# Kernel optimization log

Hardware: AMD Instinct MI355X
Metric: run time of the kernel (lower is better)

The kernel has to match this reference:

```python
import jax, jax.numpy as jnp
import numpy as np

N, C, OUT, E, H = 4096, 256, 256, 131072, 8
DH = C // H
EPS = 1e-5


def layer_norm(h, g, b):
    mu = jnp.mean(h, axis=-1, keepdims=True)
    var = jnp.mean(jnp.square(h - mu), axis=-1, keepdims=True)
    return (h - mu) * jax.lax.rsqrt(var + EPS) * g + b


def setup_inputs() -> dict:
    key = jax.random.key(0)
    ks = jax.random.split(key, 12)
    s = 1.0 / np.sqrt(C)
    return {
        "x": jax.random.normal(ks[0], (N, C), jnp.float32),
        "edge_index": jax.random.randint(ks[1], (2, E), 0, N, jnp.int32),
        "edge_attr": jax.random.normal(ks[2], (E, C), jnp.float32),
        # nn.MultiheadAttention params
        "in_proj_w": jax.random.uniform(ks[3], (3 * C, C), jnp.float32, -s, s),
        "in_proj_b": jnp.zeros((3 * C,), jnp.float32),
        "attn_out_w": jax.random.uniform(ks[4], (C, C), jnp.float32, -s, s),
        "attn_out_b": jnp.zeros((C,), jnp.float32),
        # edge_mlp: Linear(3C -> OUT) + LayerNorm(OUT)
        "edge_w": jax.random.uniform(ks[5], (OUT, 3 * C), jnp.float32, -1 / np.sqrt(3 * C), 1 / np.sqrt(3 * C)),
        "edge_b": jax.random.uniform(ks[6], (OUT,), jnp.float32, -1 / np.sqrt(3 * C), 1 / np.sqrt(3 * C)),
        "ln1_g": jnp.ones((OUT,), jnp.float32),
        "ln1_b": jnp.zeros((OUT,), jnp.float32),
        # output_proj: Linear(C + OUT -> OUT)
        "out_w": jax.random.uniform(ks[7], (OUT, C + OUT), jnp.float32, -1 / np.sqrt(C + OUT), 1 / np.sqrt(C + OUT)),
        "out_b": jax.random.uniform(ks[8], (OUT,), jnp.float32, -1 / np.sqrt(C + OUT), 1 / np.sqrt(C + OUT)),
        "ln2_g": jnp.ones((OUT,), jnp.float32),
        "ln2_b": jnp.zeros((OUT,), jnp.float32),
    }


def reference(x, edge_index, edge_attr, in_proj_w, in_proj_b, attn_out_w, attn_out_b,
              edge_w, edge_b, ln1_g, ln1_b, out_w, out_b, ln2_g, ln2_b):
    num_nodes = x.shape[0]
    # --- dense self-attention over all nodes (seq len = N, batch 1) ---
    qkv = x @ in_proj_w.T + in_proj_b            # [N, 3C]
    q, k, v = jnp.split(qkv, 3, axis=-1)
    q = q.reshape(num_nodes, H, DH).transpose(1, 0, 2)  # [H, N, DH]
    k = k.reshape(num_nodes, H, DH).transpose(1, 0, 2)
    v = v.reshape(num_nodes, H, DH).transpose(1, 0, 2)
    scores = jnp.einsum("hqd,hkd->hqk", q, k) / np.sqrt(DH)
    attn = jax.nn.softmax(scores, axis=-1)       # dropout inactive at eval
    ctx = jnp.einsum("hqk,hkd->hqd", attn, v)    # [H, N, DH]
    ctx = ctx.transpose(1, 0, 2).reshape(num_nodes, C)
    x_attn = ctx @ attn_out_w.T + attn_out_b     # [N, C]
    # --- vectorized edge messages: gather -> MLP -> scatter-add ---
    row, col = edge_index[0], edge_index[1]
    msg_in = jnp.concatenate([x[row], x[col], edge_attr], axis=-1)  # [E, 3C]
    msg = jax.nn.relu(layer_norm(msg_in @ edge_w.T + edge_b, ln1_g, ln1_b))
    node_messages = jax.ops.segment_sum(msg, col, num_segments=num_nodes)  # [N, OUT]
    # --- combine, project, residual, norm ---
    combined = jnp.concatenate([x_attn, node_messages], axis=-1)
    out = combined @ out_w.T + out_b
    out = out + x                                # OUT == C so residual fires
    return layer_norm(out, ln2_g, ln2_b)
```

## Files before the change

### kernel.cpp

```cpp
#include <hip/hip_runtime.h>
#include <hip/hip_bf16.h>
#include <math.h>

typedef __bf16 bf16;
typedef __bf16 bf16x8 __attribute__((ext_vector_type(8)));
typedef __bf16 bf16x4 __attribute__((ext_vector_type(4)));
typedef float f32x4 __attribute__((ext_vector_type(4)));

#define MFMA16(a, b, c) __builtin_amdgcn_mfma_f32_16x16x32_bf16((a), (b), (c), 0, 0, 0)

#define N_NODES 4096
#define C_DIM   256
#define E_EDGES 131072
#define APAD    280

__device__ __forceinline__ float ldf(const void* p, int i, bool f32) {
    return f32 ? ((const float*)p)[i] : (float)((const bf16*)p)[i];
}

__device__ __forceinline__ bf16x8 ld8(const void* base, size_t off, bool f32) {
    if (f32) {
        const float* p = (const float*)base + off;
        float4 a = *(const float4*)p;
        float4 b = *(const float4*)(p + 4);
        bf16x8 r;
        r[0] = (bf16)a.x; r[1] = (bf16)a.y; r[2] = (bf16)a.z; r[3] = (bf16)a.w;
        r[4] = (bf16)b.x; r[5] = (bf16)b.y; r[6] = (bf16)b.z; r[7] = (bf16)b.w;
        return r;
    }
    return *(const bf16x8*)((const bf16*)base + off);
}

__global__ __launch_bounds__(64) void detect_dtype(const void* x, int* flag)
{
    const bf16* xb = (const bf16*)x;
    int tid = threadIdx.x;
    int bad = 0;
    for (int i = tid; i < 4096; i += 64) {
        float v = fabsf((float)xb[i]);
        if (!(v >= 1e-6f && v <= 100.0f)) bad++;
    }
#pragma unroll
    for (int m = 1; m < 64; m <<= 1) bad += __shfl_xor(bad, m);
    if (tid == 0) *flag = (bad > 400) ? 1 : 0;
}

__global__ __launch_bounds__(256) void convert_inputs(
    const void* s0, const void* s1, const void* s2, const void* s3, const void* s4,
    bf16* dst, const int* flag)
{
    int idx = blockIdx.x * 256 + threadIdx.x;
    const void* src; int local;
    if (idx < 1048576)      { src = s0; local = idx; }
    else if (idx < 1245184) { src = s1; local = idx - 1048576; }
    else if (idx < 1310720) { src = s2; local = idx - 1245184; }
    else if (idx < 1507328) { src = s3; local = idx - 1310720; }
    else                    { src = s4; local = idx - 1507328; }
    if (*flag) dst[idx] = (bf16)(((const float*)src)[local]);
    else ((unsigned short*)dst)[idx] = ((const unsigned short*)src)[local];
}

__global__ __launch_bounds__(256) void edge_hist(
    const int* __restrict__ ecol, int* __restrict__ counts)
{
    int e = blockIdx.x * 256 + threadIdx.x;
    atomicAdd(&counts[ecol[e]], 1);
}

__global__ __launch_bounds__(256) void edge_scan(
    const int* __restrict__ counts, int* __restrict__ offsets,
    int* __restrict__ cursor)
{
    __shared__ int part[256];
    __shared__ int pref[257];
    int t = threadIdx.x;
    int base = t * 16;
    int s = 0;
#pragma unroll
    for (int i = 0; i < 16; ++i) s += counts[base + i];
    part[t] = s;
    __syncthreads();
    if (t == 0) {
        int run = 0;
        for (int i = 0; i < 256; ++i) { pref[i] = run; run += part[i]; }
        pref[256] = run;
    }
    __syncthreads();
    int off = pref[t];
#pragma unroll
    for (int i = 0; i < 16; ++i) {
        offsets[base + i] = off;
        cursor[base + i]  = off;
        off += counts[base + i];
    }
    if (t == 255) offsets[4096] = off;
}

__global__ __launch_bounds__(256) void edge_scatter(
    const int* __restrict__ ecol, int* __restrict__ cursor,
    int* __restrict__ eid)
{
    int e = blockIdx.x * 256 + threadIdx.x;
    int pos = atomicAdd(&cursor[ecol[e]], 1);
    eid[pos] = e;
}

__global__ __launch_bounds__(256) void gemm_bt(
    const bf16* __restrict__ A, int lda,
    const bf16* __restrict__ W, int ldw,
    const void* __restrict__ bias,
    void* __restrict__ Cout, int ldc, int c_f32,
    const bf16* __restrict__ resid, int ldr,
    int K, const int* __restrict__ flag)
{
    const bool f32 = (*flag != 0);
    const int wave = threadIdx.x >> 6;
    const int lane = threadIdx.x & 63;
    const int quad = lane >> 4;
    const int l16  = lane & 15;
    const int m_base = blockIdx.x * 32;
    const int n_base = blockIdx.y * 256 + wave * 64;

    const bf16* a0p = A + (size_t)(m_base + l16) * lda + quad * 8;
    const bf16* a1p = a0p + (size_t)16 * lda;
    const bf16* wp  = W + (size_t)(n_base + l16) * ldw + quad * 8;

    f32x4 acc[2][4] = {};
    for (int k = 0; k < K; k += 32) {
        bf16x8 a0 = *(const bf16x8*)(a0p + k);
        bf16x8 a1 = *(const bf16x8*)(a1p + k);
#pragma unroll
        for (int nt = 0; nt < 4; ++nt) {
            bf16x8 b = *(const bf16x8*)(wp + (size_t)nt * 16 * ldw + k);
            acc[0][nt] = MFMA16(a0, b, acc[0][nt]);
            acc[1][nt] = MFMA16(a1, b, acc[1][nt]);
        }
    }
#pragma unroll
    for (int mt = 0; mt < 2; ++mt) {
#pragma unroll
        for (int nt = 0; nt < 4; ++nt) {
            int col = n_base + nt * 16 + l16;
            float bv = bias ? ldf(bias, col, f32) : 0.0f;
#pragma unroll
            for (int r = 0; r < 4; ++r) {
                int row = m_base + mt * 16 + quad * 4 + r;
                float v = acc[mt][nt][r] + bv;
                if (resid) v += (float)resid[(size_t)row * ldr + col];
                if (c_f32) ((float*)Cout)[(size_t)row * ldc + col] = v;
                else       ((bf16*)Cout)[(size_t)row * ldc + col] = (bf16)v;
            }
        }
    }
}

__global__ __launch_bounds__(256) void transpose_v(
    const bf16* __restrict__ qkv, bf16* __restrict__ vt)
{
    __shared__ bf16 t[32][65];
    const int n0 = blockIdx.x * 64;
    const int c0 = blockIdx.y * 32;
    const int tid = threadIdx.x;
    {
        int cl = tid & 31, nl = tid >> 5;
#pragma unroll
        for (int p = 0; p < 8; ++p) {
            int n = nl + p * 8;
            t[cl][n] = qkv[(size_t)(n0 + n) * 768 + 512 + c0 + cl];
        }
    }
    __syncthreads();
    {
        int nn = tid & 63, cc = tid >> 6;
#pragma unroll
        for (int p = 0; p < 8; ++p) {
            int c = cc + p * 4;
            vt[(size_t)(c0 + c) * 4096 + n0 + nn] = t[c][nn];
        }
    }
}

__global__ __launch_bounds__(256) void attn_kernel(
    const bf16* __restrict__ qkv,
    const bf16* __restrict__ vt,
    bf16* __restrict__ ctx)
{
    __shared__ bf16 P[4][16][32];
    __shared__ float mL[4][16], lL[4][16];
    __shared__ float oL[4][16][32];
    const int tid  = threadIdx.x;
    const int wave = tid >> 6;
    const int lane = tid & 63;
    const int quad = lane >> 4;
    const int l16  = lane & 15;
    const int h  = blockIdx.x >> 8;
    const int qt = blockIdx.x & 255;

    const float csc = 1.4426950408889634f * 0.17677669529663687f;

    bf16x8 qf = *(const bf16x8*)(qkv + (size_t)(qt * 16 + l16) * 768 + h * 32 + quad * 8);
    const bf16* kcol = qkv + 256 + h * 32 + quad * 8;
    const bf16* vth  = vt + (size_t)h * 32 * 4096;

    float mrun[4] = {-INFINITY, -INFINITY, -INFINITY, -INFINITY};
    float lrun[4] = {0.f, 0.f, 0.f, 0.f};
    f32x4 o0 = {}, o1 = {};
    const f32x4 zero = {};

    const int kbeg = wave * 1024;
    for (int k0 = kbeg; k0 < kbeg + 1024; k0 += 32) {
        const bf16* kp = kcol + (size_t)(k0 + l16) * 768;
        bf16x8 kf0 = *(const bf16x8*)kp;
        bf16x8 kf1 = *(const bf16x8*)(kp + (size_t)16 * 768);
        f32x4 s0 = MFMA16(qf, kf0, zero);
        f32x4 s1 = MFMA16(qf, kf1, zero);

        float tm[4], p0[4], p1[4], ts[4], alpha[4], nm[4];
#pragma unroll
        for (int r = 0; r < 4; ++r) tm[r] = fmaxf(s0[r], s1[r]);
#pragma unroll
        for (int msk = 1; msk < 16; msk <<= 1) {
#pragma unroll
            for (int r = 0; r < 4; ++r) tm[r] = fmaxf(tm[r], __shfl_xor(tm[r], msk));
        }
#pragma unroll
        for (int r = 0; r < 4; ++r) {
            nm[r] = fmaxf(mrun[r], tm[r]);
            alpha[r] = exp2f((mrun[r] - nm[r]) * csc);
            p0[r] = exp2f((s0[r] - nm[r]) * csc);
            p1[r] = exp2f((s1[r] - nm[r]) * csc);
            ts[r] = p0[r] + p1[r];
        }
#pragma unroll
        for (int msk = 1; msk < 16; msk <<= 1) {
#pragma unroll
            for (int r = 0; r < 4; ++r) ts[r] += __shfl_xor(ts[r], msk);
        }
#pragma unroll
        for (int r = 0; r < 4; ++r) {
            lrun[r] = lrun[r] * alpha[r] + ts[r];
            mrun[r] = nm[r];
            o0[r] *= alpha[r];
            o1[r] *= alpha[r];
        }
        __syncthreads();
#pragma unroll
        for (int r = 0; r < 4; ++r) {
            P[wave][quad * 4 + r][l16]      = (bf16)p0[r];
            P[wave][quad * 4 + r][16 + l16] = (bf16)p1[r];
        }
        __syncthreads();
        bf16x8 pf = *(const bf16x8*)&P[wave][l16][quad * 8];
        const bf16* vp = vth + (size_t)l16 * 4096 + k0 + quad * 8;
        bf16x8 v0 = *(const bf16x8*)vp;
        bf16x8 v1 = *(const bf16x8*)(vp + (size_t)16 * 4096);
        o0 = MFMA16(pf, v0, o0);
        o1 = MFMA16(pf, v1, o1);
    }
    if (l16 == 0) {
#pragma unroll
        for (int r = 0; r < 4; ++r) {
            mL[wave][quad * 4 + r] = mrun[r];
            lL[wave][quad * 4 + r] = lrun[r];
        }
    }
#pragma unroll
    for (int r = 0; r < 4; ++r) {
        oL[wave][quad * 4 + r][l16]      = o0[r];
        oL[wave][quad * 4 + r][16 + l16] = o1[r];
    }
    __syncthreads();
    if (wave == 0) {
#pragma unroll
        for (int r = 0; r < 4; ++r) {
            int row = quad * 4 + r;
            float m0 = mL[0][row], m1 = mL[1][row], m2 = mL[2][row], m3 = mL[3][row];
            float ms = fmaxf(fmaxf(m0, m1), fmaxf(m2, m3));
            float f0 = exp2f((m0 - ms) * csc), f1 = exp2f((m1 - ms) * csc);
            float f2 = exp2f((m2 - ms) * csc), f3 = exp2f((m3 - ms) * csc);
            float ls = lL[0][row] * f0 + lL[1][row] * f1 + lL[2][row] * f2 + lL[3][row] * f3;
            float inv = 1.0f / ls;
            float a = (oL[0][row][l16] * f0 + oL[1][row][l16] * f1 +
                       oL[2][row][l16] * f2 + oL[3][row][l16] * f3) * inv;
            float b = (oL[0][row][16 + l16] * f0 + oL[1][row][16 + l16] * f1 +
                       oL[2][row][16 + l16] * f2 + oL[3][row][16 + l16] * f3) * inv;
            bf16* cp = ctx + (size_t)(qt * 16 + row) * 256 + h * 32;
            cp[l16]      = (bf16)a;
            cp[16 + l16] = (bf16)b;
        }
    }
}

__global__ __launch_bounds__(256) void edge_msg_v3(
    const int* __restrict__ erow, const int* __restrict__ ecol,
    const void* __restrict__ eattr,
    const bf16* __restrict__ ew,
    const void* __restrict__ eb,
    const void* __restrict__ g1, const void* __restrict__ b1,
    const bf16* __restrict__ U, const bf16* __restrict__ V,
    bf16* __restrict__ msg, const int* __restrict__ flag)
{
    __shared__ char smem[64 * APAD * 2];
    bf16* Asm = (bf16*)smem;
    float (*Trow)[256] = (float(*)[256])smem;

    const bool f32 = (*flag != 0);
    const int tid  = threadIdx.x;
    const int wave = tid >> 6;
    const int lane = tid & 63;
    const int quad = lane >> 4;
    const int l16  = lane & 15;
    const int e_base = blockIdx.x * 64;

    bf16x8 breg[8][4];
#pragma unroll
    for (int k0 = 0; k0 < 8; ++k0)
#pragma unroll
        for (int nt = 0; nt < 4; ++nt)
            breg[k0][nt] = *(const bf16x8*)(ew +
                (size_t)(wave * 64 + nt * 16 + l16) * 768 + 512 + k0 * 32 + quad * 8);

    {
        int row   = tid >> 2;
        int cbase = (tid & 3) * 64;
        bf16* dst = Asm + row * APAD + cbase;
        if (!f32) {
            const bf16* src = (const bf16*)eattr + (size_t)(e_base + row) * 256 + cbase;
#pragma unroll
            for (int j = 0; j < 8; ++j)
                *(bf16x8*)(dst + j * 8) = *(const bf16x8*)(src + j * 8);
        } else {
            const float* src = (const float*)eattr + (size_t)(e_base + row) * 256 + cbase;
#pragma unroll
            for (int j = 0; j < 8; ++j) {
                float4 a = *(const float4*)(src + j * 8);
                float4 b = *(const float4*)(src + j * 8 + 4);
                bf16x8 r;
                r[0] = (bf16)a.x; r[1] = (bf16)a.y; r[2] = (bf16)a.z; r[3] = (bf16)a.w;
                r[4] = (bf16)b.x; r[5] = (bf16)b.y; r[6] = (bf16)b.z; r[7] = (bf16)b.w;
                *(bf16x8*)(dst + j * 8) = r;
            }
        }
    }
    __syncthreads();

    f32x4 acc[4][4] = {};
#pragma unroll
    for (int k0 = 0; k0 < 8; ++k0) {
#pragma unroll
        for (int mt = 0; mt < 4; ++mt) {
            bf16x8 af = *(const bf16x8*)(Asm + (mt * 16 + l16) * APAD + k0 * 32 + quad * 8);
#pragma unroll
            for (int nt = 0; nt < 4; ++nt)
                acc[mt][nt] = MFMA16(af, breg[k0][nt], acc[mt][nt]);
        }
    }

    float ebv[4];
#pragma unroll
    for (int nt = 0; nt < 4; ++nt)
        ebv[nt] = ldf(eb, wave * 64 + nt * 16 + l16, f32);
    float glv[4], blv[4];
#pragma unroll
    for (int i = 0; i < 4; ++i) {
        glv[i] = ldf(g1, lane * 4 + i, f32);
        blv[i] = ldf(b1, lane * 4 + i, f32);
    }

    for (int p = 0; p < 2; ++p) {
        __syncthreads();
#pragma unroll
        for (int mtl = 0; mtl < 2; ++mtl) {
            int mt = p * 2 + mtl;
#pragma unroll
            for (int nt = 0; nt < 4; ++nt)
#pragma unroll
                for (int r = 0; r < 4; ++r)
                    Trow[mtl * 16 + quad * 4 + r][wave * 64 + nt * 16 + l16] =
                        acc[mt][nt][r] + ebv[nt];
        }
        __syncthreads();
        for (int rl = 0; rl < 8; ++rl) {
            int row = wave * 8 + rl;
            int e = e_base + p * 32 + row;
            int er = erow[e], ec = ecol[e];
            float4 t4 = *(const float4*)&Trow[row][lane * 4];
            bf16x4 u4 = *(const bf16x4*)(U + (size_t)er * 256 + lane * 4);
            bf16x4 w4 = *(const bf16x4*)(V + (size_t)ec * 256 + lane * 4);
            float v[4];
            v[0] = t4.x + (float)u4[0] + (float)w4[0];
            v[1] = t4.y + (float)u4[1] + (float)w4[1];
            v[2] = t4.z + (float)u4[2] + (float)w4[2];
            v[3] = t4.w + (float)u4[3] + (float)w4[3];
            float s = v[0] + v[1] + v[2] + v[3];
            float q = v[0]*v[0] + v[1]*v[1] + v[2]*v[2] + v[3]*v[3];
#pragma unroll
            for (int msk = 1; msk < 64; msk <<= 1) {
                s += __shfl_xor(s, msk);
                q += __shfl_xor(q, msk);
            }
            float mean = s * (1.0f / 256.0f);
            float var  = q * (1.0f / 256.0f) - mean * mean;
            float rstd = rsqrtf(var + 1e-5f);
            bf16x4 o;
#pragma unroll
            for (int i = 0; i < 4; ++i)
                o[i] = (bf16)fmaxf((v[i] - mean) * rstd * glv[i] + blv[i], 0.0f);
            *(bf16x4*)(msg + (size_t)e * 256 + lane * 4) = o;
        }
    }
}

__global__ __launch_bounds__(256) void node_gather(
    const bf16* __restrict__ msg,
    const int* __restrict__ offsets, const int* __restrict__ eid,
    bf16* __restrict__ combined)
{
    const int wave = threadIdx.x >> 6, lane = threadIdx.x & 63;
    const int node = blockIdx.x * 4 + wave;
    const int start = offsets[node];
    const int cnt   = offsets[node + 1] - start;
    float a0 = 0.f, a1 = 0.f, a2 = 0.f, a3 = 0.f;
    int i = 0;
    for (; i + 4 <= cnt; i += 4) {
        int e0 = eid[start + i],     e1 = eid[start + i + 1];
        int e2 = eid[start + i + 2], e3 = eid[start + i + 3];
        bf16x4 r0 = *(const bf16x4*)(msg + (size_t)e0 * 256 + lane * 4);
        bf16x4 r1 = *(const bf16x4*)(msg + (size_t)e1 * 256 + lane * 4);
        bf16x4 r2 = *(const bf16x4*)(msg + (size_t)e2 * 256 + lane * 4);
        bf16x4 r3 = *(const bf16x4*)(msg + (size_t)e3 * 256 + lane * 4);
        a0 += (float)r0[0] + (float)r1[0] + (float)r2[0] + (float)r3[0];
        a1 += (float)r0[1] + (float)r1[1] + (float)r2[1] + (float)r3[1];
        a2 += (float)r0[2] + (float)r1[2] + (float)r2[2] + (float)r3[2];
        a3 += (float)r0[3] + (float)r1[3] + (float)r2[3] + (float)r3[3];
    }
    for (; i < cnt; ++i) {
        int e = eid[start + i];
        bf16x4 r = *(const bf16x4*)(msg + (size_t)e * 256 + lane * 4);
        a0 += (float)r[0]; a1 += (float)r[1]; a2 += (float)r[2]; a3 += (float)r[3];
    }
    bf16* cp = combined + (size_t)node * 512 + 256 + lane * 4;
    cp[0] = (bf16)a0; cp[1] = (bf16)a1; cp[2] = (bf16)a2; cp[3] = (bf16)a3;
}

__global__ __launch_bounds__(256) void edge_node(
    const bf16* __restrict__ x,
    const int* __restrict__ erow,
    const void* __restrict__ eattr,
    const bf16* __restrict__ ew,
    const void* __restrict__ eb,
    const void* __restrict__ g1, const void* __restrict__ b1,
    const int* __restrict__ offsets, const int* __restrict__ eid,
    bf16* __restrict__ combined, const int* __restrict__ flag)
{
    __shared__ float part[32][4][2];
    const bool f32 = (*flag != 0);
    const int wave = threadIdx.x >> 6;
    const int lane = threadIdx.x & 63;
    const int quad = lane >> 4;
    const int l16  = lane & 15;
    const int n = blockIdx.x;
    const int start = offsets[n];
    const int cnt   = offsets[n + 1] - start;

    float gv[4], bv[4], ebv[4];
#pragma unroll
    for (int nt = 0; nt < 4; ++nt) {
        int col = wave * 64 + nt * 16 + l16;
        gv[nt]  = ldf(g1, col, f32);
        bv[nt]  = ldf(b1, col, f32);
        ebv[nt] = ldf(eb, col, f32);
    }
    const bf16* wp = ew + (size_t)(wave * 64 + l16) * 768 + quad * 8;
    const bf16* xn = x + (size_t)n * 256 + quad * 8;

    f32x4 acc1[4] = {};
#pragma unroll
    for (int kk = 0; kk < 8; ++kk) {
        bf16x8 a = *(const bf16x8*)(xn + kk * 32);
#pragma unroll
        for (int nt = 0; nt < 4; ++nt) {
            bf16x8 b = *(const bf16x8*)(wp + (size_t)nt * 16 * 768 + 256 + kk * 32);
            acc1[nt] = MFMA16(a, b, acc1[nt]);
        }
    }
    float nacc[4] = {0.f, 0.f, 0.f, 0.f};
    for (int c0 = 0; c0 < cnt; c0 += 32) {
        int i0 = c0 + l16;      i0 = (i0 < cnt) ? i0 : 0;
        int i1 = c0 + 16 + l16; i1 = (i1 < cnt) ? i1 : 0;
        int e0 = eid[start + i0];
        int e1 = eid[start + i1];
        const bf16* xr0 = x + (size_t)erow[e0] * 256 + quad * 8;
        const bf16* xr1 = x + (size_t)erow[e1] * 256 + quad * 8;
        f32x4 acc[2][4];
#pragma unroll
        for (int nt = 0; nt < 4; ++nt) { acc[0][nt] = acc1[nt]; acc[1][nt] = acc1[nt]; }
#pragma unroll
        for (int kk = 0; kk < 8; ++kk) {
            bf16x8 a0 = *(const bf16x8*)(xr0 + kk * 32);
            bf16x8 a1 = *(const bf16x8*)(xr1 + kk * 32);
#pragma unroll
            for (int nt = 0; nt < 4; ++nt) {
                bf16x8 b = *(const bf16x8*)(wp + (size_t)nt * 16 * 768 + kk * 32);
                acc[0][nt] = MFMA16(a0, b, acc[0][nt]);
                acc[1][nt] = MFMA16(a1, b, acc[1][nt]);
            }
        }
#pragma unroll
        for (int kk = 0; kk < 8; ++kk) {
            int koff = quad * 8 + kk * 32;
            bf16x8 a0 = ld8(eattr, (size_t)e0 * 256 + koff, f32);
            bf16x8 a1 = ld8(eattr, (size_t)e1 * 256 + koff, f32);
#pragma unroll
            for (int nt = 0; nt < 4; ++nt) {
                bf16x8 b = *(const bf16x8*)(wp + (size_t)nt * 16 * 768 + 512 + kk * 32);
                acc[0][nt] = MFMA16(a0, b, acc[0][nt]);
                acc[1][nt] = MFMA16(a1, b, acc[1][nt]);
            }
        }
#pragma unroll
        for (int mt = 0; mt < 2; ++mt)
#pragma unroll
            for (int nt = 0; nt < 4; ++nt)
#pragma unroll
                for (int r = 0; r < 4; ++r) acc[mt][nt][r] += ebv[nt];
        float ps[2][4], pq[2][4];
#pragma unroll
        for (int mt = 0; mt < 2; ++mt)
#pragma unroll
            for (int r = 0; r < 4; ++r) {
                float s = 0.f, q = 0.f;
#pragma unroll
                for (int nt = 0; nt < 4; ++nt) {
                    float v = acc[mt][nt][r];
                    s += v; q += v * v;
                }
                ps[mt][r] = s; pq[mt][r] = q;
            }
#pragma unroll
        for (int msk = 1; msk < 16; msk <<= 1)
#pragma unroll
            for (int mt = 0; mt < 2; ++mt)
#pragma unroll
                for (int r = 0; r < 4; ++r) {
                    ps[mt][r] += __shfl_xor(ps[mt][r], msk);
                    pq[mt][r] += __shfl_xor(pq[mt][r], msk);
                }
        if (l16 == 0) {
#pragma unroll
            for (int mt = 0; mt < 2; ++mt)
#pragma unroll
                for (int r = 0; r < 4; ++r) {
                    part[mt * 16 + quad * 4 + r][wave][0] = ps[mt][r];
                    part[mt * 16 + quad * 4 + r][wave][1] = pq[mt][r];
                }
        }
        __syncthreads();
#pragma unroll
        for (int mt = 0; mt < 2; ++mt)
#pragma unroll
            for (int r = 0; r < 4; ++r) {
                int row = mt * 16 + quad * 4 + r;
                float s = part[row][0][0] + part[row][1][0] + part[row][2][0] + part[row][3][0];
                float q = part[row][0][1] + part[row][1][1] + part[row][2][1] + part[row][3][1];
                float mean = s * (1.0f / 256.0f);
                float var  = q * (1.0f / 256.0f) - mean * mean;
                float rstd = rsqrtf(var + 1e-5f);
                if ((c0 + row) < cnt) {
#pragma unroll
                    for (int nt = 0; nt < 4; ++nt) {
                        float val = (acc[mt][nt][r] - mean) * rstd * gv[nt] + bv[nt];
                        nacc[nt] += fmaxf(val, 0.0f);
                    }
                }
            }
        __syncthreads();
    }
#pragma unroll
    for (int nt = 0; nt < 4; ++nt) {
        nacc[nt] += __shfl_xor(nacc[nt], 16);
        nacc[nt] += __shfl_xor(nacc[nt], 32);
    }
    if (quad == 0) {
#pragma unroll
        for (int nt = 0; nt < 4; ++nt)
            combined[(size_t)n * 512 + 256 + wave * 64 + nt * 16 + l16] = (bf16)nacc[nt];
    }
}

__global__ __launch_bounds__(256) void ln_out_kernel(
    const float* __restrict__ pre,
    const void* __restrict__ g, const void* __restrict__ bb,
    void* __restrict__ out, const int* __restrict__ flag)
{
    const bool f32 = (*flag != 0);
    const int wave = threadIdx.x >> 6, lane = threadIdx.x & 63;
    const int row = blockIdx.x * 4 + wave;
    float4 v4 = *(const float4*)(pre + (size_t)row * 256 + lane * 4);
    float v[4] = {v4.x, v4.y, v4.z, v4.w};
    float s  = v[0] + v[1] + v[2] + v[3];
    float sq = v[0]*v[0] + v[1]*v[1] + v[2]*v[2] + v[3]*v[3];
#pragma unroll
    for (int msk = 1; msk < 64; msk <<= 1) {
        s  += __shfl_xor(s, msk);
        sq += __shfl_xor(sq, msk);
    }
    float mean = s * (1.0f / 256.0f);
    float var  = sq * (1.0f / 256.0f) - mean * mean;
    float rstd = rsqrtf(var + 1e-5f);
#pragma unroll
    for (int i = 0; i < 4; ++i) {
        int c = lane * 4 + i;
        float r = (v[i] - mean) * rstd * ldf(g, c, f32) + ldf(bb, c, f32);
        if (f32) ((float*)out)[(size_t)row * 256 + c] = r;
        else     ((bf16*)out)[(size_t)row * 256 + c] = (bf16)r;
    }
}

extern "C" void kernel_launch(void* const* d_in, const int* in_sizes, int n_in,
                              void* d_out, int out_size, void* d_ws, size_t ws_size,
                              hipStream_t stream)
{
    const void* x_raw  = d_in[0];
    const int*  eidx   = (const int*)d_in[1];
    const void* eattr  = d_in[2];
    const void* in_w   = d_in[3];
    const void* in_b   = d_in[4];
    const void* ao_w   = d_in[5];
    const void* ao_b   = d_in[6];
    const void* e_w    = d_in[7];
    const void* e_b    = d_in[8];
    const void* g1     = d_in[9];
    const void* b1     = d_in[10];
    const void* o_w    = d_in[11];
    const void* o_b    = d_in[12];
    const void* g2     = d_in[13];
    const void* b2     = d_in[14];

    char* ws = (char*)d_ws;
    bf16*  qkv      = (bf16*)(ws);
    bf16*  vt       = (bf16*)(ws + 6291456);
    bf16*  ctx      = (bf16*)(ws + 8388608);
    bf16*  combined = (bf16*)(ws + 10485760);
    int*   counts   = (int*)(ws + 14680064);
    int*   offsets  = (int*)(ws + 14696448);
    int*   cursor   = (int*)(ws + 14712848);
    int*   eid      = (int*)(ws + 14729232);
    float* out_pre  = (float*)(ws + 18874368);
    bf16*  U        = (bf16*)(ws + 18874368);
    bf16*  V        = (bf16*)(ws + 20971520);
    bf16*  canon    = (bf16*)(ws + 23068672);
    int*   flag     = (int*)(ws + 26345472);
    bf16*  msg      = (bf16*)(ws + 26345728);

    const size_t WS_NEEDED = 93454592;

    bf16* x_bf   = canon;
    bf16* inw_bf = canon + 1048576;
    bf16* aow_bf = canon + 1245184;
    bf16* ew_bf  = canon + 1310720;
    bf16* ow_bf  = canon + 1507328;

    const int* erow = eidx;
    const int* ecol = eidx + E_EDGES;

    detect_dtype<<<dim3(1), 64, 0, stream>>>(x_raw, flag);
    convert_inputs<<<dim3(6400), 256, 0, stream>>>(x_raw, in_w, ao_w, e_w, o_w,
                                                   canon, flag);
    hipMemsetAsync(counts, 0, 16384, stream);
    edge_hist<<<dim3(E_EDGES / 256), 256, 0, stream>>>(ecol, counts);
    edge_scan<<<dim3(1), 256, 0, stream>>>(counts, offsets, cursor);
    edge_scatter<<<dim3(E_EDGES / 256), 256, 0, stream>>>(ecol, cursor, eid);

    gemm_bt<<<dim3(128, 1), 256, 0, stream>>>(x_bf, 256, ew_bf, 768, nullptr,
                                              U, 256, 0, nullptr, 0, 256, flag);
    gemm_bt<<<dim3(128, 1), 256, 0, stream>>>(x_bf, 256, ew_bf + 256, 768, nullptr,
                                              V, 256, 0, nullptr, 0, 256, flag);

    gemm_bt<<<dim3(128, 3), 256, 0, stream>>>(x_bf, 256, inw_bf, 256, in_b,
                                              qkv, 768, 0, nullptr, 0, 256, flag);
    transpose_v<<<dim3(64, 8), 256, 0, stream>>>(qkv, vt);
    attn_kernel<<<dim3(2048), 256, 0, stream>>>(qkv, vt, ctx);
    gemm_bt<<<dim3(128, 1), 256, 0, stream>>>(ctx, 256, aow_bf, 256, ao_b,
                                              combined, 512, 0, nullptr, 0, 256, flag);
    if (ws_size >= WS_NEEDED) {
        edge_msg_v3<<<dim3(E_EDGES / 64), 256, 0, stream>>>(erow, ecol, eattr,
                                                            ew_bf, e_b, g1, b1,
                                                            U, V, msg, flag);
        node_gather<<<dim3(N_NODES / 4), 256, 0, stream>>>(msg, offsets, eid, combined);
    } else {
        edge_node<<<dim3(N_NODES), 256, 0, stream>>>(x_bf, erow, eattr,
                                                     ew_bf, e_b, g1, b1,
                                                     offsets, eid, combined, flag);
    }
    gemm_bt<<<dim3(128, 1), 256, 0, stream>>>(combined, 512, ow_bf, 512, o_b,
                                              out_pre, 256, 1, x_bf, 256, 512, flag);
    ln_out_kernel<<<dim3(N_NODES / 4), 256, 0, stream>>>(out_pre, g2, b2, d_out, flag);
}
```

Measured before the change: 557.0 us.

## Restructure attention inner loop with 64-key steps, K prefetch, lazy rescale, swizzled P

The flash-attention loop now handles 64 keys per iteration and prefetches the next K fragments one step ahead. The row-sum reduction is deferred to the end of the loop, and the rescale is skipped unless the running max grows. Both __syncthreads in the loop are removed in favour of a per-wave XOR-swizzled LDS buffer for P, and the V transpose writes a permuted key order so the P layout matches the MFMA operand. Together these aim to cut barrier stalls, shuffle traffic and exp work. The cost is more register pressure, plus a reliance on wave-synchronous LDS access with no explicit barrier.

Result: faster. 539.6 us (-3.1%).

```diff
diff --git a/kernel.cpp b/kernel.cpp
--- a/kernel.cpp
+++ b/kernel.cpp
@@ -172,10 +172,11 @@
     __syncthreads();
     {
         int nn = tid & 63, cc = tid >> 6;
+        int np = ((nn & 15) << 2) | (nn >> 4);
 #pragma unroll
         for (int p = 0; p < 8; ++p) {
             int c = cc + p * 4;
-            vt[(size_t)(c0 + c) * 4096 + n0 + nn] = t[c][nn];
+            vt[(size_t)(c0 + c) * 4096 + n0 + np] = t[c][nn];
         }
     }
 }
@@ -185,7 +186,7 @@
     const bf16* __restrict__ vt,
     bf16* __restrict__ ctx)
 {
-    __shared__ bf16 P[4][16][32];
+    __shared__ char Psm[4][2048];
     __shared__ float mL[4][16], lL[4][16];
     __shared__ float oL[4][16][32];
     const int tid  = threadIdx.x;
@@ -200,68 +201,102 @@
 
     bf16x8 qf = *(const bf16x8*)(qkv + (size_t)(qt * 16 + l16) * 768 + h * 32 + quad * 8);
     const bf16* kcol = qkv + 256 + h * 32 + quad * 8;
-    const bf16* vth  = vt + (size_t)h * 32 * 4096;
-
-    float mrun[4] = {-INFINITY, -INFINITY, -INFINITY, -INFINITY};
-    float lrun[4] = {0.f, 0.f, 0.f, 0.f};
+    const bf16* vth  = vt + (size_t)(h * 32) * 4096;
+
+    char* Pw = Psm[wave];
+    char* pst[4];
+#pragma unroll
+    for (int r = 0; r < 4; ++r) {
+        int row = quad * 4 + r;
+        pst[r] = Pw + row * 128 + ((l16 * 8) ^ ((row & 7) << 4));
+    }
+    const char* prd0 = Pw + l16 * 128 + (((0 * 64) + quad * 16) ^ ((l16 & 7) << 4));
+    const char* prd1 = Pw + l16 * 128 + (((1 * 64) + quad * 16) ^ ((l16 & 7) << 4));
+
+    float mrun[4], lacc[4];
+#pragma unroll
+    for (int r = 0; r < 4; ++r) { mrun[r] = -INFINITY; lacc[r] = 0.f; }
     f32x4 o0 = {}, o1 = {};
     const f32x4 zero = {};
 
     const int kbeg = wave * 1024;
-    for (int k0 = kbeg; k0 < kbeg + 1024; k0 += 32) {
-        const bf16* kp = kcol + (size_t)(k0 + l16) * 768;
-        bf16x8 kf0 = *(const bf16x8*)kp;
-        bf16x8 kf1 = *(const bf16x8*)(kp + (size_t)16 * 768);
-        f32x4 s0 = MFMA16(qf, kf0, zero);
-        f32x4 s1 = MFMA16(qf, kf1, zero);
-
-        float tm[4], p0[4], p1[4], ts[4], alpha[4], nm[4];
-#pragma unroll
-        for (int r = 0; r < 4; ++r) tm[r] = fmaxf(s0[r], s1[r]);
-#pragma unroll
-        for (int msk = 1; msk < 16; msk <<= 1) {
-#pragma unroll
-            for (int r = 0; r < 4; ++r) tm[r] = fmaxf(tm[r], __shfl_xor(tm[r], msk));
-        }
+    bf16x8 kf[4];
+#pragma unroll
+    for (int t = 0; t < 4; ++t)
+        kf[t] = *(const bf16x8*)(kcol + (size_t)(kbeg + t * 16 + l16) * 768);
+
+    for (int k0 = kbeg; k0 < kbeg + 1024; k0 += 64) {
+        bf16x8 vf00 = *(const bf16x8*)(vth + (size_t)l16 * 4096 + k0 + quad * 8);
+        bf16x8 vf01 = *(const bf16x8*)(vth + (size_t)(16 + l16) * 4096 + k0 + quad * 8);
+        bf16x8 vf10 = *(const bf16x8*)(vth + (size_t)l16 * 4096 + k0 + 32 + quad * 8);
+        bf16x8 vf11 = *(const bf16x8*)(vth + (size_t)(16 + l16) * 4096 + k0 + 32 + quad * 8);
+
+        f32x4 s0 = MFMA16(qf, kf[0], zero);
+        f32x4 s1 = MFMA16(qf, kf[1], zero);
+        f32x4 s2 = MFMA16(qf, kf[2], zero);
+        f32x4 s3 = MFMA16(qf, kf[3], zero);
+
+        if (k0 + 64 < kbeg + 1024) {
+#pragma unroll
+            for (int t = 0; t < 4; ++t)
+                kf[t] = *(const bf16x8*)(kcol + (size_t)(k0 + 64 + t * 16 + l16) * 768);
+        }
+
+        float tm[4];
+#pragma unroll
+        for (int r = 0; r < 4; ++r)
+            tm[r] = fmaxf(fmaxf(s0[r], s1[r]), fmaxf(s2[r], s3[r]));
+#pragma unroll
+        for (int msk = 1; msk < 16; msk <<= 1)
+#pragma unroll
+            for (int r = 0; r < 4; ++r)
+                tm[r] = fmaxf(tm[r], __shfl_xor(tm[r], msk));
+
+        int grow = (tm[0] > mrun[0]) | (tm[1] > mrun[1]) |
+                   (tm[2] > mrun[2]) | (tm[3] > mrun[3]);
+        if (__any(grow)) {
+#pragma unroll
+            for (int r = 0; r < 4; ++r) {
+                float nm = fmaxf(mrun[r], tm[r]);
+                float al = exp2f((mrun[r] - nm) * csc);
+                mrun[r] = nm;
+                lacc[r] *= al;
+                o0[r] *= al;
+                o1[r] *= al;
+            }
+        }
+
 #pragma unroll
         for (int r = 0; r < 4; ++r) {
-            nm[r] = fmaxf(mrun[r], tm[r]);
-            alpha[r] = exp2f((mrun[r] - nm[r]) * csc);
-            p0[r] = exp2f((s0[r] - nm[r]) * csc);
-            p1[r] = exp2f((s1[r] - nm[r]) * csc);
-            ts[r] = p0[r] + p1[r];
-        }
-#pragma unroll
-        for (int msk = 1; msk < 16; msk <<= 1) {
-#pragma unroll
-            for (int r = 0; r < 4; ++r) ts[r] += __shfl_xor(ts[r], msk);
-        }
-#pragma unroll
-        for (int r = 0; r < 4; ++r) {
-            lrun[r] = lrun[r] * alpha[r] + ts[r];
-            mrun[r] = nm[r];
-            o0[r] *= alpha[r];
-            o1[r] *= alpha[r];
-        }
-        __syncthreads();
-#pragma unroll
-        for (int r = 0; r < 4; ++r) {
-            P[wave][quad * 4 + r][l16]      = (bf16)p0[r];
-            P[wave][quad * 4 + r][16 + l16] = (bf16)p1[r];
-        }
-        __syncthreads();
-        bf16x8 pf = *(const bf16x8*)&P[wave][l16][quad * 8];
-        const bf16* vp = vth + (size_t)l16 * 4096 + k0 + quad * 8;
-        bf16x8 v0 = *(const bf16x8*)vp;
-        bf16x8 v1 = *(const bf16x8*)(vp + (size_t)16 * 4096);
-        o0 = MFMA16(pf, v0, o0);
-        o1 = MFMA16(pf, v1, o1);
-    }
+            float p0 = exp2f((s0[r] - mrun[r]) * csc);
+            float p1 = exp2f((s1[r] - mrun[r]) * csc);
+            float p2 = exp2f((s2[r] - mrun[r]) * csc);
+            float p3 = exp2f((s3[r] - mrun[r]) * csc);
+            lacc[r] += (p0 + p1) + (p2 + p3);
+            bf16x4 pk;
+            pk[0] = (bf16)p0; pk[1] = (bf16)p1; pk[2] = (bf16)p2; pk[3] = (bf16)p3;
+            *(bf16x4*)pst[r] = pk;
+        }
+
+        bf16x8 pf0 = *(const bf16x8*)prd0;
+        bf16x8 pf1 = *(const bf16x8*)prd1;
+        o0 = MFMA16(pf0, vf00, o0);
+        o1 = MFMA16(pf0, vf01, o1);
+        o0 = MFMA16(pf1, vf10, o0);
+        o1 = MFMA16(pf1, vf11, o1);
+    }
+
+#pragma unroll
+    for (int msk = 1; msk < 16; msk <<= 1)
+#pragma unroll
+        for (int r = 0; r < 4; ++r)
+            lacc[r] += __shfl_xor(lacc[r], msk);
+
     if (l16 == 0) {
 #pragma unroll
         for (int r = 0; r < 4; ++r) {
             mL[wave][quad * 4 + r] = mrun[r];
-            lL[wave][quad * 4 + r] = lrun[r];
+            lL[wave][quad * 4 + r] = lacc[r];
         }
     }
 #pragma unroll
```

## Rewrite attention with 32x32 MFMA and register-resident P; restructure edge LayerNorm epilogue

Applied to the files above, without the earlier changes.

The attention kernel now uses 32x32x16 bf16 MFMA tiles over 32 queries per block. It computes S transposed so the softmax row reduction needs only one cross-half shuffle. P is packed and exchanged with v_permlane32_swap in registers instead of going through LDS with two block barriers per iteration, and the max is rescaled lazily only when it grows. The edge-message epilogue now has 8 threads per edge row with vectorized 8-wide loads and a 3-step shuffle reduction, using a padded staging tile to avoid LDS bank conflicts. These changes rely on gfx950-specific instructions and exact lane-layout assumptions.

Result: faster. 522.0 us (-6.3%).

```diff
diff --git a/kernel.cpp b/kernel.cpp
--- a/kernel.cpp
+++ b/kernel.cpp
@@ -6,13 +6,16 @@
 typedef __bf16 bf16x8 __attribute__((ext_vector_type(8)));
 typedef __bf16 bf16x4 __attribute__((ext_vector_type(4)));
 typedef float f32x4 __attribute__((ext_vector_type(4)));
+typedef float f32x16 __attribute__((ext_vector_type(16)));
 
 #define MFMA16(a, b, c) __builtin_amdgcn_mfma_f32_16x16x32_bf16((a), (b), (c), 0, 0, 0)
+#define MFMA32(a, b, c) __builtin_amdgcn_mfma_f32_32x32x16_bf16((a), (b), (c), 0, 0, 0)
 
 #define N_NODES 4096
 #define C_DIM   256
 #define E_EDGES 131072
 #define APAD    280
+#define TPAD    260
 
 __device__ __forceinline__ float ldf(const void* p, int i, bool f32) {
     return f32 ? ((const float*)p)[i] : (float)((const bf16*)p)[i];
@@ -31,6 +34,30 @@
     return *(const bf16x8*)((const bf16*)base + off);
 }
 
+__device__ __forceinline__ void ld8f(const void* base, int off, bool f32, float* o) {
+    if (f32) {
+        float4 a = *(const float4*)((const float*)base + off);
+        float4 b = *(const float4*)((const float*)base + off + 4);
+        o[0] = a.x; o[1] = a.y; o[2] = a.z; o[3] = a.w;
+        o[4] = b.x; o[5] = b.y; o[6] = b.z; o[7] = b.w;
+    } else {
+        bf16x8 r = *(const bf16x8*)((const bf16*)base + off);
+#pragma unroll
+        for (int j = 0; j < 8; ++j) o[j] = (float)r[j];
+    }
+}
+
+__device__ __forceinline__ unsigned cvtpk(float a, float b) {
+    unsigned r;
+    asm("v_cvt_pk_bf16_f32 %0, %1, %2" : "=v"(r) : "v"(a), "v"(b));
+    return r;
+}
+__device__ __forceinline__ void pl32swap(unsigned &a, unsigned &b) {
+    asm volatile("v_permlane32_swap_b32 %0, %1" : "+v"(a), "+v"(b));
+}
+
+union PW { unsigned u[4]; bf16x8 v; };
+
 __global__ __launch_bounds__(64) void detect_dtype(const void* x, int* flag)
 {
     const bf16* xb = (const bf16*)x;
@@ -185,109 +212,103 @@
     const bf16* __restrict__ vt,
     bf16* __restrict__ ctx)
 {
-    __shared__ bf16 P[4][16][32];
-    __shared__ float mL[4][16], lL[4][16];
-    __shared__ float oL[4][16][32];
+    __shared__ float oL[4][32][33];
+    __shared__ float mS[4][32];
+    __shared__ float lS[4][32];
     const int tid  = threadIdx.x;
     const int wave = tid >> 6;
     const int lane = tid & 63;
-    const int quad = lane >> 4;
-    const int l16  = lane & 15;
-    const int h  = blockIdx.x >> 8;
-    const int qt = blockIdx.x & 255;
+    const int l32  = lane & 31;
+    const int hl   = lane >> 5;
+    const int h  = blockIdx.x >> 7;
+    const int qt = blockIdx.x & 127;
 
     const float csc = 1.4426950408889634f * 0.17677669529663687f;
 
-    bf16x8 qf = *(const bf16x8*)(qkv + (size_t)(qt * 16 + l16) * 768 + h * 32 + quad * 8);
-    const bf16* kcol = qkv + 256 + h * 32 + quad * 8;
-    const bf16* vth  = vt + (size_t)h * 32 * 4096;
-
-    float mrun[4] = {-INFINITY, -INFINITY, -INFINITY, -INFINITY};
-    float lrun[4] = {0.f, 0.f, 0.f, 0.f};
-    f32x4 o0 = {}, o1 = {};
-    const f32x4 zero = {};
+    const bf16* qrow = qkv + (size_t)(qt * 32 + l32) * 768 + h * 32 + hl * 8;
+    bf16x8 qf1 = *(const bf16x8*)qrow;
+    bf16x8 qf2 = *(const bf16x8*)(qrow + 16);
+
+    const bf16* kbp = qkv + 256 + h * 32 + hl * 8;
+    const bf16* vrp = vt + (size_t)(h * 32 + l32) * 4096 + hl * 8;
+
+    float mrun = -INFINITY, msc = -INFINITY, lacc = 0.f;
+    f32x16 oacc = {};
+    const f32x16 z16 = {};
 
     const int kbeg = wave * 1024;
     for (int k0 = kbeg; k0 < kbeg + 1024; k0 += 32) {
-        const bf16* kp = kcol + (size_t)(k0 + l16) * 768;
-        bf16x8 kf0 = *(const bf16x8*)kp;
-        bf16x8 kf1 = *(const bf16x8*)(kp + (size_t)16 * 768);
-        f32x4 s0 = MFMA16(qf, kf0, zero);
-        f32x4 s1 = MFMA16(qf, kf1, zero);
-
-        float tm[4], p0[4], p1[4], ts[4], alpha[4], nm[4];
-#pragma unroll
-        for (int r = 0; r < 4; ++r) tm[r] = fmaxf(s0[r], s1[r]);
-#pragma unroll
-        for (int msk = 1; msk < 16; msk <<= 1) {
-#pragma unroll
-            for (int r = 0; r < 4; ++r) tm[r] = fmaxf(tm[r], __shfl_xor(tm[r], msk));
-        }
-#pragma unroll
-        for (int r = 0; r < 4; ++r) {
-            nm[r] = fmaxf(mrun[r], tm[r]);
-            alpha[r] = exp2f((mrun[r] - nm[r]) * csc);
-            p0[r] = exp2f((s0[r] - nm[r]) * csc);
-            p1[r] = exp2f((s1[r] - nm[r]) * csc);
-            ts[r] = p0[r] + p1[r];
-        }
-#pragma unroll
-        for (int msk = 1; msk < 16; msk <<= 1) {
-#pragma unroll
-            for (int r = 0; r < 4; ++r) ts[r] += __shfl_xor(ts[r], msk);
-        }
-#pragma unroll
-        for (int r = 0; r < 4; ++r) {
-            lrun[r] = lrun[r] * alpha[r] + ts[r];
-            mrun[r] = nm[r];
-            o0[r] *= alpha[r];
-            o1[r] *= alpha[r];
-        }
-        __syncthreads();
-#pragma unroll
-        for (int r = 0; r < 4; ++r) {
-            P[wave][quad * 4 + r][l16]      = (bf16)p0[r];
-            P[wave][quad * 4 + r][16 + l16] = (bf16)p1[r];
-        }
-        __syncthreads();
-        bf16x8 pf = *(const bf16x8*)&P[wave][l16][quad * 8];
-        const bf16* vp = vth + (size_t)l16 * 4096 + k0 + quad * 8;
-        bf16x8 v0 = *(const bf16x8*)vp;
-        bf16x8 v1 = *(const bf16x8*)(vp + (size_t)16 * 4096);
-        o0 = MFMA16(pf, v0, o0);
-        o1 = MFMA16(pf, v1, o1);
-    }
-    if (l16 == 0) {
-#pragma unroll
-        for (int r = 0; r < 4; ++r) {
-            mL[wave][quad * 4 + r] = mrun[r];
-            lL[wave][quad * 4 + r] = lrun[r];
-        }
-    }
-#pragma unroll
-    for (int r = 0; r < 4; ++r) {
-        oL[wave][quad * 4 + r][l16]      = o0[r];
-        oL[wave][quad * 4 + r][16 + l16] = o1[r];
+        const bf16* kp = kbp + (size_t)(k0 + l32) * 768;
+        bf16x8 kf1 = *(const bf16x8*)kp;
+        bf16x8 kf2 = *(const bf16x8*)(kp + 16);
+        bf16x8 vf1 = *(const bf16x8*)(vrp + k0);
+        bf16x8 vf2 = *(const bf16x8*)(vrp + k0 + 16);
+
+        f32x16 s = MFMA32(kf1, qf1, z16);
+        s = MFMA32(kf2, qf2, s);
+
+        float a0 = fmaxf(fmaxf(s[0], s[1]), fmaxf(s[2], s[3]));
+        float a1 = fmaxf(fmaxf(s[4], s[5]), fmaxf(s[6], s[7]));
+        float a2 = fmaxf(fmaxf(s[8], s[9]), fmaxf(s[10], s[11]));
+        float a3 = fmaxf(fmaxf(s[12], s[13]), fmaxf(s[14], s[15]));
+        float tm = fmaxf(fmaxf(a0, a1), fmaxf(a2, a3));
+        tm = fmaxf(tm, __shfl_xor(tm, 32));
+
+        if (__any(tm > mrun)) {
+            float nm = fmaxf(mrun, tm);
+            float nmsc = nm * csc;
+            float al = exp2f(msc - nmsc);
+            mrun = nm; msc = nmsc;
+            lacc *= al;
+#pragma unroll
+            for (int i = 0; i < 16; ++i) oacc[i] *= al;
+        }
+
+        float p[16];
+#pragma unroll
+        for (int i = 0; i < 16; ++i) {
+            p[i] = exp2f(__builtin_fmaf(s[i], csc, -msc));
+            lacc += p[i];
+        }
+
+        unsigned w0 = cvtpk(p[0], p[1]),  w1 = cvtpk(p[2], p[3]);
+        unsigned w2 = cvtpk(p[4], p[5]),  w3 = cvtpk(p[6], p[7]);
+        unsigned w4 = cvtpk(p[8], p[9]),  w5 = cvtpk(p[10], p[11]);
+        unsigned w6 = cvtpk(p[12], p[13]), w7 = cvtpk(p[14], p[15]);
+        pl32swap(w0, w2); pl32swap(w1, w3);
+        pl32swap(w4, w6); pl32swap(w5, w7);
+        PW f1; f1.u[0] = w0; f1.u[1] = w1; f1.u[2] = w2; f1.u[3] = w3;
+        PW f2; f2.u[0] = w4; f2.u[1] = w5; f2.u[2] = w6; f2.u[3] = w7;
+
+        oacc = MFMA32(vf1, f1.v, oacc);
+        oacc = MFMA32(vf2, f2.v, oacc);
+    }
+
+    lacc += __shfl_xor(lacc, 32);
+    if (hl == 0) { mS[wave][l32] = mrun; lS[wave][l32] = lacc; }
+#pragma unroll
+    for (int i = 0; i < 16; ++i) {
+        int d = (i & 3) + 8 * (i >> 2) + 4 * hl;
+        oL[wave][l32][d] = oacc[i];
     }
     __syncthreads();
-    if (wave == 0) {
-#pragma unroll
-        for (int r = 0; r < 4; ++r) {
-            int row = quad * 4 + r;
-            float m0 = mL[0][row], m1 = mL[1][row], m2 = mL[2][row], m3 = mL[3][row];
-            float ms = fmaxf(fmaxf(m0, m1), fmaxf(m2, m3));
-            float f0 = exp2f((m0 - ms) * csc), f1 = exp2f((m1 - ms) * csc);
-            float f2 = exp2f((m2 - ms) * csc), f3 = exp2f((m3 - ms) * csc);
-            float ls = lL[0][row] * f0 + lL[1][row] * f1 + lL[2][row] * f2 + lL[3][row] * f3;
-            float inv = 1.0f / ls;
-            float a = (oL[0][row][l16] * f0 + oL[1][row][l16] * f1 +
-                       oL[2][row][l16] * f2 + oL[3][row][l16] * f3) * inv;
-            float b = (oL[0][row][16 + l16] * f0 + oL[1][row][16 + l16] * f1 +
-                       oL[2][row][16 + l16] * f2 + oL[3][row][16 + l16] * f3) * inv;
-            bf16* cp = ctx + (size_t)(qt * 16 + row) * 256 + h * 32;
-            cp[l16]      = (bf16)a;
-            cp[16 + l16] = (bf16)b;
-        }
+    {
+        int q = tid >> 3, d0 = (tid & 7) * 4;
+        float m0 = mS[0][q], m1 = mS[1][q], m2 = mS[2][q], m3 = mS[3][q];
+        float ms = fmaxf(fmaxf(m0, m1), fmaxf(m2, m3));
+        float f0 = exp2f((m0 - ms) * csc), f1 = exp2f((m1 - ms) * csc);
+        float f2 = exp2f((m2 - ms) * csc), f3 = exp2f((m3 - ms) * csc);
+        float ls = lS[0][q] * f0 + lS[1][q] * f1 + lS[2][q] * f2 + lS[3][q] * f3;
+        float inv = 1.0f / ls;
+        bf16x4 o4;
+#pragma unroll
+        for (int i = 0; i < 4; ++i) {
+            int d = d0 + i;
+            float v = (oL[0][q][d] * f0 + oL[1][q][d] * f1 +
+                       oL[2][q][d] * f2 + oL[3][q][d] * f3) * inv;
+            o4[i] = (bf16)v;
+        }
+        *(bf16x4*)(ctx + (size_t)(qt * 32 + q) * 256 + h * 32 + d0) = o4;
     }
 }
 
@@ -302,7 +323,7 @@
 {
     __shared__ char smem[64 * APAD * 2];
     bf16* Asm = (bf16*)smem;
-    float (*Trow)[256] = (float(*)[256])smem;
+    float (*Trow)[TPAD] = (float(*)[TPAD])smem;
 
     const bool f32 = (*flag != 0);
     const int tid  = threadIdx.x;
@@ -360,12 +381,6 @@
 #pragma unroll
     for (int nt = 0; nt < 4; ++nt)
         ebv[nt] = ldf(eb, wave * 64 + nt * 16 + l16, f32);
-    float glv[4], blv[4];
-#pragma unroll
-    for (int i = 0; i < 4; ++i) {
-        glv[i] = ldf(g1, lane * 4 + i, f32);
-        blv[i] = ldf(b1, lane * 4 + i, f32);
-    }
 
     for (int p = 0; p < 2; ++p) {
         __syncthreads();
@@ -380,33 +395,58 @@
                         acc[mt][nt][r] + ebv[nt];
         }
         __syncthreads();
-        for (int rl = 0; rl < 8; ++rl) {
-            int row = wave * 8 + rl;
+        {
+            int row = tid >> 3;
+            int seg = tid & 7;
             int e = e_base + p * 32 + row;
             int er = erow[e], ec = ecol[e];
-            float4 t4 = *(const float4*)&Trow[row][lane * 4];
-            bf16x4 u4 = *(const bf16x4*)(U + (size_t)er * 256 + lane * 4);
-            bf16x4 w4 = *(const bf16x4*)(V + (size_t)ec * 256 + lane * 4);
-            float v[4];
-            v[0] = t4.x + (float)u4[0] + (float)w4[0];
-            v[1] = t4.y + (float)u4[1] + (float)w4[1];
-            v[2] = t4.z + (float)u4[2] + (float)w4[2];
-            v[3] = t4.w + (float)u4[3] + (float)w4[3];
-            float s = v[0] + v[1] + v[2] + v[3];
-            float q = v[0]*v[0] + v[1]*v[1] + v[2]*v[2] + v[3]*v[3];
-#pragma unroll
-            for (int msk = 1; msk < 64; msk <<= 1) {
+            const float* tr = &Trow[row][seg * 32];
+            const bf16* up = U + (size_t)er * 256 + seg * 32;
+            const bf16* wp = V + (size_t)ec * 256 + seg * 32;
+            float v[32];
+            float s = 0.f, q = 0.f;
+#pragma unroll
+            for (int i = 0; i < 4; ++i) {
+                float4 ta = *(const float4*)(tr + i * 8);
+                float4 tb = *(const float4*)(tr + i * 8 + 4);
+                bf16x8 u8 = *(const bf16x8*)(up + i * 8);
+                bf16x8 w8 = *(const bf16x8*)(wp + i * 8);
+                float t0 = ta.x + (float)u8[0] + (float)w8[0];
+                float t1 = ta.y + (float)u8[1] + (float)w8[1];
+                float t2 = ta.z + (float)u8[2] + (float)w8[2];
+                float t3 = ta.w + (float)u8[3] + (float)w8[3];
+                float t4 = tb.x + (float)u8[4] + (float)w8[4];
+                float t5 = tb.y + (float)u8[5] + (float)w8[5];
+                float t6 = tb.z + (float)u8[6] + (float)w8[6];
+                float t7 = tb.w + (float)u8[7] + (float)w8[7];
+                v[i*8+0] = t0; v[i*8+1] = t1; v[i*8+2] = t2; v[i*8+3] = t3;
+                v[i*8+4] = t4; v[i*8+5] = t5; v[i*8+6] = t6; v[i*8+7] = t7;
+                s += ((t0 + t1) + (t2 + t3)) + ((t4 + t5) + (t6 + t7));
+                q = __builtin_fmaf(t0, t0, q); q = __builtin_fmaf(t1, t1, q);
+                q = __builtin_fmaf(t2, t2, q); q = __builtin_fmaf(t3, t3, q);
+                q = __builtin_fmaf(t4, t4, q); q = __builtin_fmaf(t5, t5, q);
+                q = __builtin_fmaf(t6, t6, q); q = __builtin_fmaf(t7, t7, q);
+            }
+#pragma unroll
+            for (int msk = 1; msk < 8; msk <<= 1) {
                 s += __shfl_xor(s, msk);
                 q += __shfl_xor(q, msk);
             }
             float mean = s * (1.0f / 256.0f);
             float var  = q * (1.0f / 256.0f) - mean * mean;
             float rstd = rsqrtf(var + 1e-5f);
-            bf16x4 o;
-#pragma unroll
-            for (int i = 0; i < 4; ++i)
-                o[i] = (bf16)fmaxf((v[i] - mean) * rstd * glv[i] + blv[i], 0.0f);
-            *(bf16x4*)(msg + (size_t)e * 256 + lane * 4) = o;
+            bf16* op = msg + (size_t)e * 256 + seg * 32;
+#pragma unroll
+            for (int i = 0; i < 4; ++i) {
+                float gv[8], bv[8];
+                ld8f(g1, seg * 32 + i * 8, f32, gv);
+                ld8f(b1, seg * 32 + i * 8, f32, bv);
+                bf16x8 o8;
+#pragma unroll
+                for (int j = 0; j < 8; ++j)
+                    o8[j] = (bf16)fmaxf((v[i*8+j] - mean) * rstd * gv[j] + bv[j], 0.0f);
+                *(bf16x8*)(op + i * 8) = o8;
+            }
         }
     }
 }
@@ -680,7 +720,7 @@
     gemm_bt<<<dim3(128, 3), 256, 0, stream>>>(x_bf, 256, inw_bf, 256, in_b,
                                               qkv, 768, 0, nullptr, 0, 256, flag);
     transpose_v<<<dim3(64, 8), 256, 0, stream>>>(qkv, vt);
-    attn_kernel<<<dim3(2048), 256, 0, stream>>>(qkv, vt, ctx);
+    attn_kernel<<<dim3(1024), 256, 0, stream>>>(qkv, vt, ctx);
     gemm_bt<<<dim3(128, 1), 256, 0, stream>>>(ctx, 256, aow_bf, 256, ao_b,
                                               combined, 512, 0, nullptr, 0, 256, flag);
     if (ws_size >= WS_NEEDED) {
```
